# Kernel optimization log

Measured on AMD Instinct MI355X. Metric: run time of the kernel, lower is better.

Reference implementation:

```python
import math
import jax, jax.numpy as jnp
import numpy as np

NUM_HEADS = 16
EMBED = 1024
B, T = 2, 2048


def setup_inputs() -> dict:
    key = jax.random.key(0)
    k1, k2 = jax.random.split(key)
    x = jax.random.normal(k1, (B, T, EMBED), dtype=jnp.float32)
    # kaiming-uniform-style init for [num_heads*embed, embed]
    bound = 1.0 / math.sqrt(NUM_HEADS * EMBED)
    weight = jax.random.uniform(k2, (NUM_HEADS * EMBED, EMBED), dtype=jnp.float32,
                                minval=-bound, maxval=bound)
    return {"x": x, "weight": weight}


def reference(x, weight):
    b, t, c = x.shape
    nh = NUM_HEADS
    hs = c // nh
    # b t (nh hs) -> b nh t hs
    y = x.reshape(b, t, nh, hs).transpose(0, 2, 1, 3)
    # scores: [b, nh, t, t], scaled by sqrt(hs) (yt.shape[-2] == hs)
    scores = jnp.einsum('bhtk,bhsk->bhts', y, y) / math.sqrt(hs)
    attn = jax.nn.softmax(scores, axis=-1)
    # value is raw x broadcast per head; contract without materializing the repeat
    o = jnp.einsum('bhts,bsc->bhtc', attn, x)          # [b, nh, t, c]
    o = o.transpose(0, 2, 1, 3).reshape(b, t, nh * c)  # b nh t c -> b t (nh c)
    return o @ weight                                   # [b, t, c]
```

## Files before the change

### kernel.cpp

```cpp
#include <hip/hip_runtime.h>
#include <hip/hip_bf16.h>


typedef __hip_bfloat16 bf16;
typedef __bf16 bf16x8 __attribute__((ext_vector_type(8)));
typedef float f32x4 __attribute__((ext_vector_type(4)));

#define B_ 2
#define T_ 2048
#define C_ 1024
#define H_ 16
#define D_ 16384
#define E_ 1024
#define KZ_ 8

__device__ __forceinline__ void load_lds16(const void* g, void* l) {
  __builtin_amdgcn_global_load_lds(
      (const __attribute__((address_space(1))) void*)g,
      (__attribute__((address_space(3))) void*)l, 16, 0, 0);
}

__device__ __forceinline__ unsigned pack2(float a, float b) {
  union { bf16 h[2]; unsigned u; } p;
  p.h[0] = __float2bfloat16(a);
  p.h[1] = __float2bfloat16(b);
  return p.u;
}

__global__ __launch_bounds__(256) void transpose_cast_kernel(
    const float* __restrict__ in, bf16* __restrict__ out, int rows, int cols) {
  __shared__ float tile[32][33];
  size_t zoff = (size_t)blockIdx.z * rows * cols;
  int c0 = blockIdx.x * 32, r0 = blockIdx.y * 32;
  int tx = threadIdx.x, ty = threadIdx.y;
  for (int i = ty; i < 32; i += 8)
    tile[i][tx] = in[zoff + (size_t)(r0 + i) * cols + c0 + tx];
  __syncthreads();
  for (int i = ty; i < 32; i += 8)
    out[zoff + (size_t)(c0 + i) * rows + r0 + tx] = __float2bfloat16(tile[tx][i]);
}

__global__ __launch_bounds__(256) void xh_cast_kernel(
    const float* __restrict__ x, bf16* __restrict__ xh) {
  int bt = blockIdx.x;
  int b = bt >> 11, t = bt & (T_ - 1);
  float4 v = ((const float4*)(x + (size_t)bt * C_))[threadIdx.x];
  int c = threadIdx.x * 4;
  int h = c >> 6, k = c & 63;
  bf16* o = xh + ((size_t)(b * H_ + h) * T_ + t) * 64 + k;
  o[0] = __float2bfloat16(v.x);
  o[1] = __float2bfloat16(v.y);
  o[2] = __float2bfloat16(v.z);
  o[3] = __float2bfloat16(v.w);
}

__global__ __launch_bounds__(256) void reduce_kernel(
    const bf16* __restrict__ p, float* __restrict__ out, int n8) {
  int i = blockIdx.x * 256 + threadIdx.x;
  if (i >= n8) return;
  float a[8] = {};
#pragma unroll
  for (int z = 0; z < KZ_; ++z) {
    bf16x8 v = ((const bf16x8*)(p + (size_t)z * n8 * 8))[i];
#pragma unroll
    for (int k = 0; k < 8; ++k) a[k] += (float)v[k];
  }
  float4 lo = make_float4(a[0], a[1], a[2], a[3]);
  float4 hi = make_float4(a[4], a[5], a[6], a[7]);
  ((float4*)out)[2 * i] = lo;
  ((float4*)out)[2 * i + 1] = hi;
}

__global__ __launch_bounds__(256) void scores_kernel(
    const bf16* __restrict__ xh,
    bf16* __restrict__ P,
    float* __restrict__ lsum) {
  int L = blockIdx.x;
  int z = blockIdx.y;
  int ti = 0, rem = L;
  while (rem >= H_ - ti) { rem -= H_ - ti; ++ti; }
  int tj = ti + rem;

  const bf16* A = xh + (size_t)z * T_ * 64;
  bf16* Pz = P + (size_t)z * T_ * T_;
  size_t row0 = (size_t)ti * 128, col0 = (size_t)tj * 128;

  __shared__ bf16 lds_a[128 * 64];
  __shared__ bf16 lds_b[128 * 64];
  int t = threadIdx.x;

  const bf16* ga = A + (row0 + (t >> 3)) * 64 + (t & 7) * 8;
  const bf16* gb = A + (col0 + (t >> 3)) * 64 + (t & 7) * 8;
#pragma unroll
  for (int q = 0; q < 4; ++q) {
    load_lds16(ga + q * 32 * 64, lds_a + t * 8 + q * 2048);
    load_lds16(gb + q * 32 * 64, lds_b + t * 8 + q * 2048);
  }
  __syncthreads();

  int lane = t & 63, w = t >> 6;
  int wm = (w & 1) * 64, wn = (w >> 1) * 64;
  int lr = lane & 15, lq = lane >> 4;
  const int a_off = (wm + lr) * 64 + lq * 8;
  const int b_off = (wn + lr) * 64 + lq * 8;

  f32x4 acc[4][4] = {};
#pragma unroll
  for (int kh = 0; kh < 2; ++kh) {
    bf16x8 af[4], bfr[4];
#pragma unroll
    for (int i = 0; i < 4; ++i)
      af[i] = *(const bf16x8*)&lds_a[a_off + kh * 32 + i * 16 * 64];
#pragma unroll
    for (int j = 0; j < 4; ++j)
      bfr[j] = *(const bf16x8*)&lds_b[b_off + kh * 32 + j * 16 * 64];
#pragma unroll
    for (int i = 0; i < 4; ++i)
#pragma unroll
      for (int j = 0; j < 4; ++j)
        acc[i][j] = __builtin_amdgcn_mfma_f32_16x16x32_bf16(af[i], bfr[j],
                                                            acc[i][j], 0, 0, 0);
  }

  float rs[4][4];
  float cs[4];
#pragma unroll
  for (int i2 = 0; i2 < 4; ++i2)
#pragma unroll
    for (int reg = 0; reg < 4; ++reg) rs[i2][reg] = 0.f;
#pragma unroll
  for (int j2 = 0; j2 < 4; ++j2) cs[j2] = 0.f;

#pragma unroll
  for (int i2 = 0; i2 < 4; ++i2) {
    size_t rb = row0 + wm + i2 * 16 + lq * 4;
#pragma unroll
    for (int j2 = 0; j2 < 4; ++j2) {
      size_t c = col0 + wn + j2 * 16 + lr;
      float e[4];
#pragma unroll
      for (int reg = 0; reg < 4; ++reg) {
        e[reg] = __expf(acc[i2][j2][reg] * 0.125f);
        rs[i2][reg] += e[reg];
        cs[j2] += e[reg];
        float nb = __shfl_xor(e[reg], 1);
        if ((lr & 1) == 0)
          *(unsigned*)&Pz[(rb + reg) * T_ + c] = pack2(e[reg], nb);
      }
      uint2 mv;
      mv.x = pack2(e[0], e[1]);
      mv.y = pack2(e[2], e[3]);
      *(uint2*)&Pz[c * T_ + rb] = mv;
    }
  }

#pragma unroll
  for (int i2 = 0; i2 < 4; ++i2)
#pragma unroll
    for (int reg = 0; reg < 4; ++reg) {
#pragma unroll
      for (int off = 1; off < 16; off <<= 1)
        rs[i2][reg] += __shfl_xor(rs[i2][reg], off);
    }
  if (lr == 0) {
#pragma unroll
    for (int i2 = 0; i2 < 4; ++i2) {
      size_t rb = row0 + wm + i2 * 16 + lq * 4;
#pragma unroll
      for (int reg = 0; reg < 4; ++reg)
        atomicAdd(&lsum[(size_t)z * T_ + rb + reg], rs[i2][reg]);
    }
  }
  if (ti != tj) {
#pragma unroll
    for (int j2 = 0; j2 < 4; ++j2) {
      cs[j2] += __shfl_xor(cs[j2], 16);
      cs[j2] += __shfl_xor(cs[j2], 32);
    }
    if (lq == 0) {
#pragma unroll
      for (int j2 = 0; j2 < 4; ++j2) {
        size_t c = col0 + wn + j2 * 16 + lr;
        atomicAdd(&lsum[(size_t)z * T_ + c], cs[j2]);
      }
    }
  }
}

template <int IH, int JH>
__device__ __forceinline__ void quad(f32x4 (&acc)[8][4], const bf16x8 (&aR)[8],
                                     const bf16x8 (&bR)[4]) {
#pragma unroll
  for (int i = 0; i < 4; ++i)
#pragma unroll
    for (int jj = 0; jj < 2; ++jj)
#pragma unroll
      for (int kk = 0; kk < 2; ++kk)
        acc[IH * 4 + i][JH * 2 + jj] = __builtin_amdgcn_mfma_f32_16x16x32_bf16(
            aR[i * 2 + kk], bR[jj * 2 + kk], acc[IH * 4 + i][JH * 2 + jj], 0, 0,
            0);
}

#define STAGE_A(bufi, h, tau)                                                 \
  do {                                                                        \
    load_lds16(Ab + offA[(h)*2 + 0] + (tau)*64,                               \
               &ldsA[bufi][(((h)*512) + t) * 8]);                             \
    load_lds16(Ab + offA[(h)*2 + 1] + (tau)*64,                               \
               &ldsA[bufi][((1024 + (h)*512) + t) * 8]);                      \
  } while (0)

#define STAGE_B(bufi, h, tau)                                                 \
  do {                                                                        \
    load_lds16(Bb + offB[(h)*2 + 0] + (tau)*64,                               \
               &ldsB[bufi][(((t >> 8) * 512) + (h)*256 + (t & 255)) * 8]);    \
    load_lds16(                                                               \
        Bb + offB[(h)*2 + 1] + (tau)*64,                                      \
        &ldsB[bufi][((((t + 512) >> 8) * 512) + (h)*256 + (t & 255)) * 8]);   \
  } while (0)

#define RD_A(dst, d, add)                                                     \
  do {                                                                        \
    dst[0] = *(const bf16x8*)&ldsA[d][aoff[0] + (add)];                       \
    dst[1] = *(const bf16x8*)&ldsA[d][aoff[1] + (add)];                       \
    dst[2] = *(const bf16x8*)&ldsA[d][aoff[2] + (add)];                       \
    dst[3] = *(const bf16x8*)&ldsA[d][aoff[3] + (add)];                       \
    dst[4] = *(const bf16x8*)&ldsA[d][aoff[4] + (add)];                       \
    dst[5] = *(const bf16x8*)&ldsA[d][aoff[5] + (add)];                       \
    dst[6] = *(const bf16x8*)&ldsA[d][aoff[6] + (add)];                       \
    dst[7] = *(const bf16x8*)&ldsA[d][aoff[7] + (add)];                       \
  } while (0)

#define RD_B(dst, d, add)                                                     \
  do {                                                                        \
    dst[0] = *(const bf16x8*)&ldsB[d][boff[0] + (add)];                       \
    dst[1] = *(const bf16x8*)&ldsB[d][boff[1] + (add)];                       \
    dst[2] = *(const bf16x8*)&ldsB[d][boff[2] + (add)];                       \
    dst[3] = *(const bf16x8*)&ldsB[d][boff[3] + (add)];                       \
  } while (0)

template <int MODE, int SWZ>
__global__ __launch_bounds__(512, 2) void gemm256_kernel(
    const bf16* __restrict__ A, long long a_zstride, int lda,
    const bf16* __restrict__ BT, long long b_zstride, int ldb,
    void* __restrict__ Cout, int ldc, long long c_zflat,
    const float* __restrict__ lsum, int lzs, int K) {
  __shared__ __align__(16) bf16 ldsA[2][256 * 64];
  __shared__ __align__(16) bf16 ldsB[2][256 * 64];
  const int t = threadIdx.x;

  int bx = blockIdx.x, by = blockIdx.y, bz = blockIdx.z;
  if (SWZ) {
    int gx = gridDim.x, gy = gridDim.y, gz = gridDim.z;
    int S = gy * gz, nb = gx * S;
    if (((S & 7) == 0) && ((nb & 7) == 0)) {
      int L = bx + gx * (by + gy * bz);
      int xcd = L & 7, m = L >> 3, spx = S >> 3;
      int col = m % gx, sl = m / gx;
      int strip = xcd * spx + sl;
      bx = col; by = strip % gy; bz = strip / gy;
    }
  }

  const bf16* Ab = A + (size_t)bz * a_zstride;
  const bf16* Bb = BT + (size_t)bz * b_zstride;
  const size_t row0 = (size_t)by * 256;
  const size_t col0 = (size_t)bx * 256;
  const int NT = K >> 6;

  int offA[4], offB[4];
#pragma unroll
  for (int h = 0; h < 2; ++h)
#pragma unroll
    for (int l = 0; l < 2; ++l) {
      int s = h * 512 + l * 1024 + t;
      int src = s ^ ((s >> 3) & 7);
      offA[h * 2 + l] =
          (int)((row0 + (size_t)(src >> 3)) * (size_t)lda) + (src & 7) * 8;
      int u = t + l * 512;
      int sb = (u >> 8) * 512 + h * 256 + (u & 255);
      int srcb = sb ^ ((sb >> 3) & 7);
      offB[h * 2 + l] =
          (int)((col0 + (size_t)(srcb >> 3)) * (size_t)ldb) + (srcb & 7) * 8;
    }

  const int lane = t & 63, w = t >> 6;
  const int wr = w >> 2, wc = w & 3;
  const int lr = lane & 15, lq = lane >> 4;
  const int axor = (lr & 7) << 3;
  int aoff[8], boff[4];
#pragma unroll
  for (int i = 0; i < 4; ++i)
#pragma unroll
    for (int kk = 0; kk < 2; ++kk)
      aoff[i * 2 + kk] =
          (((wr * 128 + i * 16 + lr) * 64) + kk * 32 + lq * 8) ^ axor;
#pragma unroll
  for (int j = 0; j < 2; ++j)
#pragma unroll
    for (int kk = 0; kk < 2; ++kk)
      boff[j * 2 + kk] =
          (((wc * 64 + j * 16 + lr) * 64) + kk * 32 + lq * 8) ^ axor;

  f32x4 acc[8][4] = {};
  bf16x8 aR[8], bR0[4], bR1[4];

  {
    const int t1 = (NT > 1) ? 1 : 0;
    STAGE_A(0, 0, 0);
    STAGE_B(0, 0, 0);
    STAGE_B(0, 1, 0);
    STAGE_A(0, 1, 0);
    STAGE_A(1, 0, t1);
    STAGE_B(1, 0, t1);
    STAGE_B(1, 1, t1);
    asm volatile("s_waitcnt vmcnt(6)" ::: "memory");
    __builtin_amdgcn_s_barrier();
  }

  for (int tt = 0; tt < NT; ++tt) {
    const int d = tt & 1, dn = d ^ 1;
    const int tp1 = (tt + 1 < NT) ? (tt + 1) : (NT - 1);
    const int tp2 = (tt + 2 < NT) ? (tt + 2) : (NT - 1);
    RD_B(bR0, d, 0);
    RD_A(aR, d, 0);
    __builtin_amdgcn_s_barrier();
    __builtin_amdgcn_s_setprio(1);
    quad<0, 0>(acc, aR, bR0);
    __builtin_amdgcn_s_setprio(0);
    STAGE_A(dn, 1, tp1);
    RD_B(bR1, d, 2048);
    __builtin_amdgcn_s_barrier();
    __builtin_amdgcn_s_setprio(1);
    quad<0, 1>(acc, aR, bR1);
    __builtin_amdgcn_s_setprio(0);
    STAGE_A(d, 0, tp2);
    RD_A(aR, d, 4096);
    __builtin_amdgcn_s_barrier();
    __builtin_amdgcn_s_setprio(1);
    quad<1, 1>(acc, aR, bR1);
    __builtin_amdgcn_s_setprio(0);
    STAGE_B(d, 0, tp2);
    __builtin_amdgcn_s_barrier();
    __builtin_amdgcn_s_setprio(1);
    quad<1, 0>(acc, aR, bR0);
    __builtin_amdgcn_s_setprio(0);
    STAGE_B(d, 1, tp2);
    asm volatile("s_waitcnt vmcnt(6)" ::: "memory");
    __builtin_amdgcn_s_barrier();
  }
  asm volatile("s_waitcnt vmcnt(0)" ::: "memory");

  size_t cbase = (size_t)bz * c_zflat + col0 + wc * 64;
#pragma unroll
  for (int i = 0; i < 8; ++i) {
    size_t r = row0 + wr * 128 + i * 16 + lq * 4;
    float4 inv4 = make_float4(1.f, 1.f, 1.f, 1.f);
    if (MODE == 3) {
      float4 lv = *(const float4*)&lsum[(size_t)bz * lzs + r];
      inv4 = make_float4(1.f / lv.x, 1.f / lv.y, 1.f / lv.z, 1.f / lv.w);
    }
#pragma unroll
    for (int j = 0; j < 4; ++j) {
      size_t c = cbase + j * 16 + lr;
#pragma unroll
      for (int reg = 0; reg < 4; ++reg) {
        float v = acc[i][j][reg];
        if (MODE == 3) {
          float iv = reg == 0 ? inv4.x : reg == 1 ? inv4.y : reg == 2 ? inv4.z
                                                                      : inv4.w;
          v *= iv;
        }
        float nb = __shfl_xor(v, 1);
        if ((lr & 1) == 0) {
          size_t idx = (r + reg) * (size_t)ldc + c;
          *(unsigned*)&((bf16*)Cout)[idx] = pack2(v, nb);
        }
      }
    }
  }
}

extern "C" void kernel_launch(void* const* d_in, const int* in_sizes, int n_in,
                              void* d_out, int out_size, void* d_ws,
                              size_t ws_size, hipStream_t stream) {
  const float* x = (const float*)d_in[0];
  const float* wgt = (const float*)d_in[1];
  float* out = (float*)d_out;

  bf16* xbT = (bf16*)d_ws;
  bf16* wbT = xbT + (size_t)B_ * C_ * T_;
  bf16* xh = wbT + (size_t)E_ * D_;
  bf16* Obuf = xh + (size_t)B_ * H_ * T_ * 64;
  float* lsum = (float*)(Obuf + (size_t)B_ * T_ * D_);
  bf16* P = (bf16*)(lsum + (size_t)16 * T_);
  bf16* partials = P;

  transpose_cast_kernel<<<dim3(C_ / 32, T_ / 32, B_), dim3(32, 8), 0, stream>>>(
      x, xbT, T_, C_);
  transpose_cast_kernel<<<dim3(E_ / 32, D_ / 32, 1), dim3(32, 8), 0, stream>>>(
      wgt, wbT, D_, E_);
  xh_cast_kernel<<<B_ * T_, 256, 0, stream>>>(x, xh);

  size_t fixed_bytes = ((size_t)B_ * C_ * T_ + (size_t)E_ * D_ +
                        (size_t)B_ * H_ * T_ * 64 + (size_t)B_ * T_ * D_) * 2 +
                       (size_t)16 * T_ * 4;
  int Hs = 16;
  while (Hs > 1 && fixed_bytes + (size_t)Hs * T_ * T_ * 2 > ws_size) Hs >>= 1;

  for (int b = 0; b < B_; ++b) {
    for (int h0 = 0; h0 < H_; h0 += Hs) {
      const bf16* xhb = xh + (size_t)(b * H_ + h0) * T_ * 64;
      hipMemsetAsync(lsum, 0, (size_t)Hs * T_ * sizeof(float), stream);
      scores_kernel<<<dim3(136, Hs), 256, 0, stream>>>(xhb, P, lsum);
      gemm256_kernel<3, 1><<<dim3(C_ / 256, T_ / 256, Hs), 512, 0, stream>>>(
          P, (long long)T_ * T_, T_, xbT + (size_t)b * C_ * T_, 0LL, T_,
          (void*)(Obuf + (size_t)b * T_ * D_ + (size_t)h0 * C_), D_,
          (long long)C_, lsum, T_, T_);
    }
  }
  gemm256_kernel<1, 1><<<dim3(E_ / 256, (B_ * T_) / 256, KZ_), 512, 0,
                         stream>>>(Obuf, (long long)(D_ / KZ_), D_, wbT,
                                   (long long)(D_ / KZ_), D_, (void*)partials,
                                   E_, (long long)B_ * T_ * E_, nullptr, 0,
                                   D_ / KZ_);
  reduce_kernel<<<(B_ * T_ * E_ / 8 + 255) / 256, 256, 0, stream>>>(
      partials, out, B_ * T_ * E_ / 8);
}
```

Measured before the change: 733.3 us.

## Load B operand directly from global into registers, dropping B LDS staging

The B tile is no longer staged through shared memory. Each wave now loads its B fragments straight from global memory into registers, which halves LDS usage and removes the B LDS writes and reads. A is now prefetched only one stage ahead instead of two, and every iteration waits on vmcnt(0). The cost is that each of the two wave rows fetches the same B data separately from global memory, the B loads are uncoalesced 16-byte strided reads, and the shallower pipeline exposes more global memory latency.

After: 929.5 us. 1.27x slower.

```diff
diff --git a/kernel.cpp b/kernel.cpp
--- a/kernel.cpp
+++ b/kernel.cpp
@@ -209,15 +209,6 @@
                &ldsA[bufi][((1024 + (h)*512) + t) * 8]);                      \
   } while (0)
 
-#define STAGE_B(bufi, h, tau)                                                 \
-  do {                                                                        \
-    load_lds16(Bb + offB[(h)*2 + 0] + (tau)*64,                               \
-               &ldsB[bufi][(((t >> 8) * 512) + (h)*256 + (t & 255)) * 8]);    \
-    load_lds16(                                                               \
-        Bb + offB[(h)*2 + 1] + (tau)*64,                                      \
-        &ldsB[bufi][((((t + 512) >> 8) * 512) + (h)*256 + (t & 255)) * 8]);   \
-  } while (0)
-
 #define RD_A(dst, d, add)                                                     \
   do {                                                                        \
     dst[0] = *(const bf16x8*)&ldsA[d][aoff[0] + (add)];                       \
@@ -230,12 +221,12 @@
     dst[7] = *(const bf16x8*)&ldsA[d][aoff[7] + (add)];                       \
   } while (0)
 
-#define RD_B(dst, d, add)                                                     \
+#define LOAD_B(dst, base0, base1, tau)                                        \
   do {                                                                        \
-    dst[0] = *(const bf16x8*)&ldsB[d][boff[0] + (add)];                       \
-    dst[1] = *(const bf16x8*)&ldsB[d][boff[1] + (add)];                       \
-    dst[2] = *(const bf16x8*)&ldsB[d][boff[2] + (add)];                       \
-    dst[3] = *(const bf16x8*)&ldsB[d][boff[3] + (add)];                       \
+    dst[0] = *(const bf16x8*)(base0 + (size_t)(tau)*64);                      \
+    dst[1] = *(const bf16x8*)(base0 + (size_t)(tau)*64 + 32);                 \
+    dst[2] = *(const bf16x8*)(base1 + (size_t)(tau)*64);                      \
+    dst[3] = *(const bf16x8*)(base1 + (size_t)(tau)*64 + 32);                 \
   } while (0)
 
 template <int MODE, int SWZ>
@@ -245,7 +236,6 @@
     void* __restrict__ Cout, int ldc, long long c_zflat,
     const float* __restrict__ lsum, int lzs, int K) {
   __shared__ __align__(16) bf16 ldsA[2][256 * 64];
-  __shared__ __align__(16) bf16 ldsB[2][256 * 64];
   const int t = threadIdx.x;
 
   int bx = blockIdx.x, by = blockIdx.y, bz = blockIdx.z;
@@ -267,7 +257,7 @@
   const size_t col0 = (size_t)bx * 256;
   const int NT = K >> 6;
 
-  int offA[4], offB[4];
+  int offA[4];
 #pragma unroll
   for (int h = 0; h < 2; ++h)
 #pragma unroll
@@ -276,79 +266,65 @@
       int src = s ^ ((s >> 3) & 7);
       offA[h * 2 + l] =
           (int)((row0 + (size_t)(src >> 3)) * (size_t)lda) + (src & 7) * 8;
-      int u = t + l * 512;
-      int sb = (u >> 8) * 512 + h * 256 + (u & 255);
-      int srcb = sb ^ ((sb >> 3) & 7);
-      offB[h * 2 + l] =
-          (int)((col0 + (size_t)(srcb >> 3)) * (size_t)ldb) + (srcb & 7) * 8;
     }
 
   const int lane = t & 63, w = t >> 6;
   const int wr = w >> 2, wc = w & 3;
   const int lr = lane & 15, lq = lane >> 4;
   const int axor = (lr & 7) << 3;
-  int aoff[8], boff[4];
+  int aoff[8];
 #pragma unroll
   for (int i = 0; i < 4; ++i)
 #pragma unroll
     for (int kk = 0; kk < 2; ++kk)
       aoff[i * 2 + kk] =
           (((wr * 128 + i * 16 + lr) * 64) + kk * 32 + lq * 8) ^ axor;
-#pragma unroll
-  for (int j = 0; j < 2; ++j)
-#pragma unroll
-    for (int kk = 0; kk < 2; ++kk)
-      boff[j * 2 + kk] =
-          (((wc * 64 + j * 16 + lr) * 64) + kk * 32 + lq * 8) ^ axor;
+
+  const bf16* pB00 = Bb + (col0 + wc * 64 + 0 + lr) * (size_t)ldb + lq * 8;
+  const bf16* pB01 = Bb + (col0 + wc * 64 + 16 + lr) * (size_t)ldb + lq * 8;
+  const bf16* pB10 = Bb + (col0 + wc * 64 + 32 + lr) * (size_t)ldb + lq * 8;
+  const bf16* pB11 = Bb + (col0 + wc * 64 + 48 + lr) * (size_t)ldb + lq * 8;
 
   f32x4 acc[8][4] = {};
   bf16x8 aR[8], bR0[4], bR1[4];
 
   {
-    const int t1 = (NT > 1) ? 1 : 0;
     STAGE_A(0, 0, 0);
-    STAGE_B(0, 0, 0);
-    STAGE_B(0, 1, 0);
     STAGE_A(0, 1, 0);
-    STAGE_A(1, 0, t1);
-    STAGE_B(1, 0, t1);
-    STAGE_B(1, 1, t1);
-    asm volatile("s_waitcnt vmcnt(6)" ::: "memory");
+    LOAD_B(bR0, pB00, pB01, 0);
+    LOAD_B(bR1, pB10, pB11, 0);
+    asm volatile("s_waitcnt vmcnt(0)" ::: "memory");
     __builtin_amdgcn_s_barrier();
   }
 
   for (int tt = 0; tt < NT; ++tt) {
     const int d = tt & 1, dn = d ^ 1;
     const int tp1 = (tt + 1 < NT) ? (tt + 1) : (NT - 1);
-    const int tp2 = (tt + 2 < NT) ? (tt + 2) : (NT - 1);
-    RD_B(bR0, d, 0);
     RD_A(aR, d, 0);
     __builtin_amdgcn_s_barrier();
     __builtin_amdgcn_s_setprio(1);
     quad<0, 0>(acc, aR, bR0);
     __builtin_amdgcn_s_setprio(0);
-    STAGE_A(dn, 1, tp1);
-    RD_B(bR1, d, 2048);
+    STAGE_A(dn, 0, tp1);
     __builtin_amdgcn_s_barrier();
     __builtin_amdgcn_s_setprio(1);
     quad<0, 1>(acc, aR, bR1);
     __builtin_amdgcn_s_setprio(0);
-    STAGE_A(d, 0, tp2);
+    STAGE_A(dn, 1, tp1);
     RD_A(aR, d, 4096);
     __builtin_amdgcn_s_barrier();
     __builtin_amdgcn_s_setprio(1);
     quad<1, 1>(acc, aR, bR1);
     __builtin_amdgcn_s_setprio(0);
-    STAGE_B(d, 0, tp2);
+    LOAD_B(bR1, pB10, pB11, tp1);
     __builtin_amdgcn_s_barrier();
     __builtin_amdgcn_s_setprio(1);
     quad<1, 0>(acc, aR, bR0);
     __builtin_amdgcn_s_setprio(0);
-    STAGE_B(d, 1, tp2);
-    asm volatile("s_waitcnt vmcnt(6)" ::: "memory");
-    __builtin_amdgcn_s_barrier();
-  }
-  asm volatile("s_waitcnt vmcnt(0)" ::: "memory");
+    LOAD_B(bR0, pB00, pB01, tp1);
+    asm volatile("s_waitcnt vmcnt(0)" ::: "memory");
+    __builtin_amdgcn_s_barrier();
+  }
 
   size_t cbase = (size_t)bz * c_zflat + col0 + wc * 64;
 #pragma unroll
```

## Restructure GEMM main loop into two phases with full A fragments in registers

Applied to the files above, without the earlier changes.

The main-loop pipeline goes from four barrier-separated MFMA quadrants per K-step to two phases. Both A halves (aLo/aHi) are read into registers up front, so each B fragment load serves two quadrants, and the prefetch schedule and vmcnt waits are re-timed to match. The aim is to cut barriers and stalls per iteration. In exchange the kernel holds more VGPRs, which may lower occupancy, and the new stage ordering must still be race-free. Tau offsets are also widened to size_t.

Measured after the change: 734.8 us. No clear change (+0.2%).

```diff
diff --git a/kernel.cpp b/kernel.cpp
--- a/kernel.cpp
+++ b/kernel.cpp
@@ -203,18 +203,18 @@
 
 #define STAGE_A(bufi, h, tau)                                                 \
   do {                                                                        \
-    load_lds16(Ab + offA[(h)*2 + 0] + (tau)*64,                               \
+    load_lds16(Ab + offA[(h)*2 + 0] + (size_t)(tau)*64,                       \
                &ldsA[bufi][(((h)*512) + t) * 8]);                             \
-    load_lds16(Ab + offA[(h)*2 + 1] + (tau)*64,                               \
+    load_lds16(Ab + offA[(h)*2 + 1] + (size_t)(tau)*64,                       \
                &ldsA[bufi][((1024 + (h)*512) + t) * 8]);                      \
   } while (0)
 
 #define STAGE_B(bufi, h, tau)                                                 \
   do {                                                                        \
-    load_lds16(Bb + offB[(h)*2 + 0] + (tau)*64,                               \
+    load_lds16(Bb + offB[(h)*2 + 0] + (size_t)(tau)*64,                       \
                &ldsB[bufi][(((t >> 8) * 512) + (h)*256 + (t & 255)) * 8]);    \
     load_lds16(                                                               \
-        Bb + offB[(h)*2 + 1] + (tau)*64,                                      \
+        Bb + offB[(h)*2 + 1] + (size_t)(tau)*64,                              \
         &ldsB[bufi][((((t + 512) >> 8) * 512) + (h)*256 + (t & 255)) * 8]);   \
   } while (0)
 
@@ -302,18 +302,17 @@
           (((wc * 64 + j * 16 + lr) * 64) + kk * 32 + lq * 8) ^ axor;
 
   f32x4 acc[8][4] = {};
-  bf16x8 aR[8], bR0[4], bR1[4];
+  bf16x8 aLo[8], aHi[8], bR[4];
 
   {
     const int t1 = (NT > 1) ? 1 : 0;
     STAGE_A(0, 0, 0);
+    STAGE_A(0, 1, 0);
     STAGE_B(0, 0, 0);
     STAGE_B(0, 1, 0);
-    STAGE_A(0, 1, 0);
     STAGE_A(1, 0, t1);
     STAGE_B(1, 0, t1);
-    STAGE_B(1, 1, t1);
-    asm volatile("s_waitcnt vmcnt(6)" ::: "memory");
+    asm volatile("s_waitcnt vmcnt(4)" ::: "memory");
     __builtin_amdgcn_s_barrier();
   }
 
@@ -321,31 +320,25 @@
     const int d = tt & 1, dn = d ^ 1;
     const int tp1 = (tt + 1 < NT) ? (tt + 1) : (NT - 1);
     const int tp2 = (tt + 2 < NT) ? (tt + 2) : (NT - 1);
-    RD_B(bR0, d, 0);
-    RD_A(aR, d, 0);
+    STAGE_B(dn, 1, tp1);
+    RD_B(bR, d, 0);
+    RD_A(aLo, d, 0);
+    RD_A(aHi, d, 4096);
     __builtin_amdgcn_s_barrier();
     __builtin_amdgcn_s_setprio(1);
-    quad<0, 0>(acc, aR, bR0);
+    quad<0, 0>(acc, aLo, bR);
+    quad<1, 0>(acc, aHi, bR);
     __builtin_amdgcn_s_setprio(0);
     STAGE_A(dn, 1, tp1);
-    RD_B(bR1, d, 2048);
+    RD_B(bR, d, 2048);
     __builtin_amdgcn_s_barrier();
     __builtin_amdgcn_s_setprio(1);
-    quad<0, 1>(acc, aR, bR1);
+    quad<0, 1>(acc, aLo, bR);
+    quad<1, 1>(acc, aHi, bR);
     __builtin_amdgcn_s_setprio(0);
     STAGE_A(d, 0, tp2);
-    RD_A(aR, d, 4096);
-    __builtin_amdgcn_s_barrier();
-    __builtin_amdgcn_s_setprio(1);
-    quad<1, 1>(acc, aR, bR1);
-    __builtin_amdgcn_s_setprio(0);
     STAGE_B(d, 0, tp2);
-    __builtin_amdgcn_s_barrier();
-    __builtin_amdgcn_s_setprio(1);
-    quad<1, 0>(acc, aR, bR0);
-    __builtin_amdgcn_s_setprio(0);
-    STAGE_B(d, 1, tp2);
-    asm volatile("s_waitcnt vmcnt(6)" ::: "memory");
+    asm volatile("s_waitcnt vmcnt(4)" ::: "memory");
     __builtin_amdgcn_s_barrier();
   }
   asm volatile("s_waitcnt vmcnt(0)" ::: "memory");
```

## Compute full score rows per block instead of symmetric tiles, drop atomics and memset

Applied to the files above, without the earlier changes.

The scores kernel stops exploiting the symmetry of Y·Yᵀ with triangular tile pairs and mirrored transposed stores. Each 512-thread block now owns a 128-row strip, loops over all 16 column tiles, and reads operands straight from global memory without LDS staging. Row sums are combined in shared memory and written directly, which removes the atomics and the lsum memset. The price is roughly double the score MFMA and exp work in exchange for coalesced row-major writes only. The split-K factor of the output projection also drops from 8 to 4, and some stage offsets are cast to size_t.

Result: slower. 786.8 us (+7.3%).

```diff
diff --git a/kernel.cpp b/kernel.cpp
--- a/kernel.cpp
+++ b/kernel.cpp
@@ -12,7 +12,7 @@
 #define H_ 16
 #define D_ 16384
 #define E_ 1024
-#define KZ_ 8
+#define KZ_ 4
 
 __device__ __forceinline__ void load_lds16(const void* g, void* l) {
   __builtin_amdgcn_global_load_lds(
@@ -71,120 +71,90 @@
   ((float4*)out)[2 * i + 1] = hi;
 }
 
-__global__ __launch_bounds__(256) void scores_kernel(
+__global__ __launch_bounds__(512) void scores_kernel(
     const bf16* __restrict__ xh,
     bf16* __restrict__ P,
     float* __restrict__ lsum) {
-  int L = blockIdx.x;
   int z = blockIdx.y;
-  int ti = 0, rem = L;
-  while (rem >= H_ - ti) { rem -= H_ - ti; ++ti; }
-  int tj = ti + rem;
-
+  size_t row0 = (size_t)blockIdx.x * 128;
   const bf16* A = xh + (size_t)z * T_ * 64;
   bf16* Pz = P + (size_t)z * T_ * T_;
-  size_t row0 = (size_t)ti * 128, col0 = (size_t)tj * 128;
-
-  __shared__ bf16 lds_a[128 * 64];
-  __shared__ bf16 lds_b[128 * 64];
-  int t = threadIdx.x;
-
-  const bf16* ga = A + (row0 + (t >> 3)) * 64 + (t & 7) * 8;
-  const bf16* gb = A + (col0 + (t >> 3)) * 64 + (t & 7) * 8;
-#pragma unroll
-  for (int q = 0; q < 4; ++q) {
-    load_lds16(ga + q * 32 * 64, lds_a + t * 8 + q * 2048);
-    load_lds16(gb + q * 32 * 64, lds_b + t * 8 + q * 2048);
+
+  int t = threadIdx.x, lane = t & 63, w = t >> 6;
+  int wm = (w & 1) * 64;
+  int wn = (w >> 1) * 32;
+  int lr = lane & 15, lq = lane >> 4;
+
+  bf16x8 af[4][2];
+#pragma unroll
+  for (int i = 0; i < 4; ++i)
+#pragma unroll
+    for (int kh = 0; kh < 2; ++kh)
+      af[i][kh] = *(const bf16x8*)&A[(row0 + wm + i * 16 + lr) * 64 + kh * 32 +
+                                     lq * 8];
+
+  float rs[4][4];
+#pragma unroll
+  for (int i = 0; i < 4; ++i)
+#pragma unroll
+    for (int reg = 0; reg < 4; ++reg) rs[i][reg] = 0.f;
+
+  for (int tj = 0; tj < 16; ++tj) {
+    size_t col0 = (size_t)tj * 128 + wn;
+    bf16x8 bfr[2][2];
+#pragma unroll
+    for (int j = 0; j < 2; ++j)
+#pragma unroll
+      for (int kh = 0; kh < 2; ++kh)
+        bfr[j][kh] = *(const bf16x8*)&A[(col0 + j * 16 + lr) * 64 + kh * 32 +
+                                        lq * 8];
+    f32x4 acc[4][2] = {};
+#pragma unroll
+    for (int i = 0; i < 4; ++i)
+#pragma unroll
+      for (int j = 0; j < 2; ++j)
+#pragma unroll
+        for (int kh = 0; kh < 2; ++kh)
+          acc[i][j] = __builtin_amdgcn_mfma_f32_16x16x32_bf16(
+              af[i][kh], bfr[j][kh], acc[i][j], 0, 0, 0);
+#pragma unroll
+    for (int i = 0; i < 4; ++i) {
+      size_t rb = row0 + wm + i * 16 + lq * 4;
+#pragma unroll
+      for (int j = 0; j < 2; ++j) {
+        size_t c = col0 + j * 16 + lr;
+#pragma unroll
+        for (int reg = 0; reg < 4; ++reg) {
+          float e = __expf(acc[i][j][reg] * 0.125f);
+          rs[i][reg] += e;
+          float nb = __shfl_xor(e, 1);
+          if ((lr & 1) == 0)
+            *(unsigned*)&Pz[(rb + reg) * T_ + c] = pack2(e, nb);
+        }
+      }
+    }
+  }
+
+#pragma unroll
+  for (int i = 0; i < 4; ++i)
+#pragma unroll
+    for (int reg = 0; reg < 4; ++reg) {
+#pragma unroll
+      for (int off = 1; off < 16; off <<= 1)
+        rs[i][reg] += __shfl_xor(rs[i][reg], off);
+    }
+  __shared__ float sbuf[4][128];
+  if (lr == 0) {
+#pragma unroll
+    for (int i = 0; i < 4; ++i)
+#pragma unroll
+      for (int reg = 0; reg < 4; ++reg)
+        sbuf[w >> 1][wm + i * 16 + lq * 4 + reg] = rs[i][reg];
   }
   __syncthreads();
-
-  int lane = t & 63, w = t >> 6;
-  int wm = (w & 1) * 64, wn = (w >> 1) * 64;
-  int lr = lane & 15, lq = lane >> 4;
-  const int a_off = (wm + lr) * 64 + lq * 8;
-  const int b_off = (wn + lr) * 64 + lq * 8;
-
-  f32x4 acc[4][4] = {};
-#pragma unroll
-  for (int kh = 0; kh < 2; ++kh) {
-    bf16x8 af[4], bfr[4];
-#pragma unroll
-    for (int i = 0; i < 4; ++i)
-      af[i] = *(const bf16x8*)&lds_a[a_off + kh * 32 + i * 16 * 64];
-#pragma unroll
-    for (int j = 0; j < 4; ++j)
-      bfr[j] = *(const bf16x8*)&lds_b[b_off + kh * 32 + j * 16 * 64];
-#pragma unroll
-    for (int i = 0; i < 4; ++i)
-#pragma unroll
-      for (int j = 0; j < 4; ++j)
-        acc[i][j] = __builtin_amdgcn_mfma_f32_16x16x32_bf16(af[i], bfr[j],
-                                                            acc[i][j], 0, 0, 0);
-  }
-
-  float rs[4][4];
-  float cs[4];
-#pragma unroll
-  for (int i2 = 0; i2 < 4; ++i2)
-#pragma unroll
-    for (int reg = 0; reg < 4; ++reg) rs[i2][reg] = 0.f;
-#pragma unroll
-  for (int j2 = 0; j2 < 4; ++j2) cs[j2] = 0.f;
-
-#pragma unroll
-  for (int i2 = 0; i2 < 4; ++i2) {
-    size_t rb = row0 + wm + i2 * 16 + lq * 4;
-#pragma unroll
-    for (int j2 = 0; j2 < 4; ++j2) {
-      size_t c = col0 + wn + j2 * 16 + lr;
-      float e[4];
-#pragma unroll
-      for (int reg = 0; reg < 4; ++reg) {
-        e[reg] = __expf(acc[i2][j2][reg] * 0.125f);
-        rs[i2][reg] += e[reg];
-        cs[j2] += e[reg];
-        float nb = __shfl_xor(e[reg], 1);
-        if ((lr & 1) == 0)
-          *(unsigned*)&Pz[(rb + reg) * T_ + c] = pack2(e[reg], nb);
-      }
-      uint2 mv;
-      mv.x = pack2(e[0], e[1]);
-      mv.y = pack2(e[2], e[3]);
-      *(uint2*)&Pz[c * T_ + rb] = mv;
-    }
-  }
-
-#pragma unroll
-  for (int i2 = 0; i2 < 4; ++i2)
-#pragma unroll
-    for (int reg = 0; reg < 4; ++reg) {
-#pragma unroll
-      for (int off = 1; off < 16; off <<= 1)
-        rs[i2][reg] += __shfl_xor(rs[i2][reg], off);
-    }
-  if (lr == 0) {
-#pragma unroll
-    for (int i2 = 0; i2 < 4; ++i2) {
-      size_t rb = row0 + wm + i2 * 16 + lq * 4;
-#pragma unroll
-      for (int reg = 0; reg < 4; ++reg)
-        atomicAdd(&lsum[(size_t)z * T_ + rb + reg], rs[i2][reg]);
-    }
-  }
-  if (ti != tj) {
-#pragma unroll
-    for (int j2 = 0; j2 < 4; ++j2) {
-      cs[j2] += __shfl_xor(cs[j2], 16);
-      cs[j2] += __shfl_xor(cs[j2], 32);
-    }
-    if (lq == 0) {
-#pragma unroll
-      for (int j2 = 0; j2 < 4; ++j2) {
-        size_t c = col0 + wn + j2 * 16 + lr;
-        atomicAdd(&lsum[(size_t)z * T_ + c], cs[j2]);
-      }
-    }
-  }
+  if (t < 128)
+    lsum[(size_t)z * T_ + row0 + t] =
+        sbuf[0][t] + sbuf[1][t] + sbuf[2][t] + sbuf[3][t];
 }
 
 template <int IH, int JH>
@@ -203,18 +173,18 @@
 
 #define STAGE_A(bufi, h, tau)                                                 \
   do {                                                                        \
-    load_lds16(Ab + offA[(h)*2 + 0] + (tau)*64,                               \
+    load_lds16(Ab + offA[(h)*2 + 0] + (size_t)(tau)*64,                       \
                &ldsA[bufi][(((h)*512) + t) * 8]);                             \
-    load_lds16(Ab + offA[(h)*2 + 1] + (tau)*64,                               \
+    load_lds16(Ab + offA[(h)*2 + 1] + (size_t)(tau)*64,                       \
                &ldsA[bufi][((1024 + (h)*512) + t) * 8]);                      \
   } while (0)
 
 #define STAGE_B(bufi, h, tau)                                                 \
   do {                                                                        \
-    load_lds16(Bb + offB[(h)*2 + 0] + (tau)*64,                               \
+    load_lds16(Bb + offB[(h)*2 + 0] + (size_t)(tau)*64,                       \
                &ldsB[bufi][(((t >> 8) * 512) + (h)*256 + (t & 255)) * 8]);    \
     load_lds16(                                                               \
-        Bb + offB[(h)*2 + 1] + (tau)*64,                                      \
+        Bb + offB[(h)*2 + 1] + (size_t)(tau)*64,                              \
         &ldsB[bufi][((((t + 512) >> 8) * 512) + (h)*256 + (t & 255)) * 8]);   \
   } while (0)
 
@@ -410,8 +380,7 @@
   for (int b = 0; b < B_; ++b) {
     for (int h0 = 0; h0 < H_; h0 += Hs) {
       const bf16* xhb = xh + (size_t)(b * H_ + h0) * T_ * 64;
-      hipMemsetAsync(lsum, 0, (size_t)Hs * T_ * sizeof(float), stream);
-      scores_kernel<<<dim3(136, Hs), 256, 0, stream>>>(xhb, P, lsum);
+      scores_kernel<<<dim3(T_ / 128, Hs), 512, 0, stream>>>(xhb, P, lsum);
       gemm256_kernel<3, 1><<<dim3(C_ / 256, T_ / 256, Hs), 512, 0, stream>>>(
           P, (long long)T_ * T_, T_, xbT + (size_t)b * C_ * T_, 0LL, T_,
           (void*)(Obuf + (size_t)b * T_ * D_ + (size_t)h0 * C_), D_,
```
